# Kernel optimization log

Hardware: AMD Instinct MI355X
Metric: run time of the kernel (lower is better)

The kernel has to match this reference:

```python
import jax, jax.numpy as jnp
import numpy as np

BLOCK = 64
THRESH = 0.95
EPS = 1e-8


def setup_inputs() -> dict:
    key = jax.random.key(0)
    kq, kk, kv = jax.random.split(key, 3)
    S, D = 4096, 128
    q = jax.random.normal(kq, (S, D), dtype=jnp.float32)
    k = jax.random.normal(kk, (S, D), dtype=jnp.float32)
    v = jax.random.normal(kv, (S, D), dtype=jnp.float32)
    return {"q": q, "k": k, "v": v}


def reference(q, k, v):
    S, D = q.shape
    nb = S // BLOCK
    qb = q.reshape(nb, BLOCK, D)
    kb = k.reshape(nb, BLOCK, D)
    vb = v.reshape(nb, BLOCK, D)
    # all block-pair scores: [nb_q, nb_k, BLOCK_q, BLOCK_k]
    scores = jnp.einsum('ibd,jcd->ijbc', qb, kb)
    m = jnp.max(scores, axis=-1, keepdims=True)
    e = jnp.exp(scores - m)
    s = jnp.sum(e, axis=-1, keepdims=True)  # per-block-pair softmax denominator
    # top-p truncation mask: sort descending, cumsum, threshold
    srt = jnp.sort(e, axis=-1)[..., ::-1]
    cum = jnp.cumsum(srt, axis=-1)
    mask = cum < THRESH * s
    # NOTE: faithful to original — mask (in sorted order) is applied to the
    # UNSORTED exp_scores, exactly as the torch code does (indices unused).
    em = e * mask
    em = em / (jnp.sum(em, axis=-1, keepdims=True) + EPS)
    # accumulate over key blocks j (per-pair normalized weights, summed)
    out = jnp.einsum('ijbc,jcd->ibd', em, vb)
    return out.reshape(S, D)
```

## Files before the change

kernel.cpp:

```cpp
#include <hip/hip_runtime.h>
#include <cstdint>
#include <cstddef>


#define SEQ   4096
#define DIM   128
#define BLK   64
#define NB    (SEQ / BLK)
#define NJG   16
#define JPB   (NB / NJG)
#define NT    256
#define PSTR  12288
#define THRESH 0.95f
#define EPSF   1e-8f

typedef __attribute__((ext_vector_type(8))) _Float16 f16x8;
typedef __attribute__((ext_vector_type(4))) float    f32x4;

#define MFMAH(a, b, c) __builtin_amdgcn_mfma_f32_16x16x32_f16((a), (b), (c), 0, 0, 0)

union UH4 { uint2 u; _Float16 h[4]; };
union UH8 { uint4 u; f16x8 v; };

__device__ __forceinline__ void gll16(const uint* g, uint* l) {
  __builtin_amdgcn_global_load_lds(
      (const __attribute__((address_space(1))) void*)g,
      (__attribute__((address_space(3))) void*)l, 16, 0, 0);
}

__global__ __launch_bounds__(NT, 4) void eco_prep_kernel(
    const float* __restrict__ K, const float* __restrict__ V,
    uint* __restrict__ P, float* __restrict__ O) {
  const int tid  = threadIdx.x;
  const int b    = blockIdx.x;
  const int jb   = b >> 2;
  const int part = b & 3;

  {
    float4 z = {0.f, 0.f, 0.f, 0.f};
    float4* op = (float4*)O;
#pragma unroll
    for (int it = 0; it < 2; ++it) op[b * 512 + it * NT + tid] = z;
  }

  {
    const float4* gk = (const float4*)(K + (size_t)jb * BLK * DIM);
    uint* dst = P + (size_t)jb * PSTR;
#pragma unroll
    for (int it = 0; it < 2; ++it) {
      int f = part * 512 + it * NT + tid;
      int r = f >> 5, c4 = f & 31;
      float4 x = gk[f];
      float xs[4] = {x.x, x.y, x.z, x.w};
      UH4 uh, ur;
#pragma unroll
      for (int e = 0; e < 4; ++e) {
        float v = xs[e];
        _Float16 h = (_Float16)v;
        uh.h[e] = h;
        ur.h[e] = (_Float16)(v - (float)h);
      }
      uint off = (uint)r * 64u + (((uint)(c4 >> 1) ^ (uint)(r & 15)) << 2) +
                 (uint)((c4 & 1) << 1);
      *(uint2*)&dst[off]        = uh.u;
      *(uint2*)&dst[4096 + off] = ur.u;
    }
  }

  {
    const float* gv = V + (size_t)jb * BLK * DIM;
    uint4* dv = (uint4*)(P + (size_t)jb * PSTR + 8192);
    int idx = part * 256 + tid;
    int ch = idx >> 7, d = idx & 127;
    UH8 u;
#pragma unroll
    for (int j = 0; j < 8; ++j)
      u.v[j] = (_Float16)gv[(ch * 8 + j) * DIM + d];
    dv[idx] = u.u;
  }
}

#define CE(x, y, dmax) { float _hi = fmaxf((x), (y)); float _lo = fminf((x), (y)); \
                         (x) = (dmax) ? _hi : _lo; (y) = (dmax) ? _lo : _hi; }

__global__ __launch_bounds__(NT, 4) void eco_attn_kernel(
    const float* __restrict__ Q, const uint* __restrict__ P,
    float* __restrict__ O) {
  __shared__ __align__(16) uint sK[8192];
  __shared__ __align__(16) uint sW[2048];

  const int tid  = threadIdx.x;
  const int ib   = blockIdx.y;
  const int jg   = blockIdx.x;
  const int lane = tid & 63;
  const int wv   = tid >> 6;
  const int quad = lane >> 4;
  const int l16  = lane & 15;
  const int q4   = quad << 2;

  uint* sWw = sW + wv * 512;

  f16x8 qh[4], qr[4];
  {
    const float* qp = Q + (size_t)(ib * BLK + wv * 16 + l16) * DIM + quad * 8;
#pragma unroll
    for (int ks = 0; ks < 4; ++ks) {
      float4 x0 = *(const float4*)(qp + ks * 32);
      float4 x1 = *(const float4*)(qp + ks * 32 + 4);
      float xs[8] = {x0.x, x0.y, x0.z, x0.w, x1.x, x1.y, x1.z, x1.w};
      f16x8 h8, r8;
#pragma unroll
      for (int e = 0; e < 8; ++e) {
        float v = xs[e];
        _Float16 h = (_Float16)v;
        h8[e] = h;
        r8[e] = (_Float16)(v - (float)h);
      }
      qh[ks] = h8; qr[ks] = r8;
    }
  }

  const f32x4 zf = {0.f, 0.f, 0.f, 0.f};
  f32x4 pv[8];
#pragma unroll
  for (int i = 0; i < 8; ++i) pv[i] = zf;

  {
    const uint* gsrc = P + (size_t)(jg * JPB) * PSTR;
#pragma unroll
    for (int it = 0; it < 8; ++it) {
      int idx = (it * NT + tid) << 2;
      gll16(gsrc + idx, sK + idx);
    }
  }

  for (int jj = 0; jj < JPB; ++jj) {
    const int jb = jg * JPB + jj;
    __syncthreads();

    f32x4 ah[4], ar[4];
#pragma unroll
    for (int nt = 0; nt < 4; ++nt) { ah[nt] = zf; ar[nt] = zf; }
#pragma unroll
    for (int nt = 0; nt < 4; ++nt) {
      const int rB = nt * 16 + l16;
      const uint rowoff = (uint)rB * 64u;
      const uint swk = (uint)(rB & 15);
#pragma unroll
      for (int ks = 0; ks < 4; ++ks) {
        uint off = rowoff + ((((uint)(ks * 4 + quad)) ^ swk) << 2);
        f16x8 bh = *(const f16x8*)&sK[off];
        f16x8 br = *(const f16x8*)&sK[4096 + off];
        ah[nt] = MFMAH(bh, qh[ks], ah[nt]);
        ar[nt] = MFMAH(br, qh[ks], ar[nt]);
        ar[nt] = MFMAH(bh, qr[ks], ar[nt]);
      }
    }
    __syncthreads();

    if (jj + 1 < JPB) {
      const uint* gsrc = P + (size_t)(jb + 1) * PSTR;
#pragma unroll
      for (int it = 0; it < 8; ++it) {
        int idx = (it * NT + tid) << 2;
        gll16(gsrc + idx, sK + idx);
      }
    }

    bool doHi;

    {
      float a[16], e[16];
#pragma unroll
      for (int nt = 0; nt < 4; ++nt) {
        f32x4 sc = ah[nt] + ar[nt];
#pragma unroll
        for (int rg = 0; rg < 4; ++rg) a[nt * 4 + rg] = sc[rg];
      }
      float mt[8];
#pragma unroll
      for (int i = 0; i < 8; ++i) mt[i] = fmaxf(a[i], a[i + 8]);
#pragma unroll
      for (int w2 = 4; w2 >= 1; w2 >>= 1)
#pragma unroll
        for (int i = 0; i < w2; ++i) mt[i] = fmaxf(mt[i], mt[i + w2]);
      float m = mt[0];
      m = fmaxf(m, __shfl_xor(m, 16, 64));
      m = fmaxf(m, __shfl_xor(m, 32, 64));
#pragma unroll
      for (int i = 0; i < 16; ++i) { a[i] = __expf(a[i] - m); e[i] = a[i]; }
      float st[8];
#pragma unroll
      for (int i = 0; i < 8; ++i) st[i] = a[i] + a[i + 8];
#pragma unroll
      for (int w2 = 4; w2 >= 1; w2 >>= 1)
#pragma unroll
        for (int i = 0; i < w2; ++i) st[i] += st[i + w2];
      float sr = st[0];
      sr += __shfl_xor(sr, 16, 64);
      sr += __shfl_xor(sr, 32, 64);
      const float T = THRESH * sr;

      float cum = 1.0f;
      bool live = (cum < T);
      int t = live ? 1 : 0;
#pragma unroll
      for (int i = 0; i < 16; ++i) a[i] = (a[i] >= 1.0f) ? 0.f : a[i];
#pragma unroll
      for (int p4 = 0; p4 < 4; ++p4) {
        float M = fmaxf(fmaxf(fmaxf(a[0], a[1]), a[2]),
                        fmaxf(fmaxf(a[3], a[4]), a[5]));
        M = fmaxf(M, fmaxf(fmaxf(a[6],  a[7]),  a[8]));
        M = fmaxf(M, fmaxf(fmaxf(a[9],  a[10]), a[11]));
        M = fmaxf(M, fmaxf(fmaxf(a[12], a[13]), a[14]));
        M = fmaxf(M, a[15]);
        M = fmaxf(M, __shfl_xor(M, 16, 64));
        M = fmaxf(M, __shfl_xor(M, 32, 64));
        const float cn = cum + M;
        const bool cross = !(cn < T) || !(M > 0.f);
        if (live) { cum = cn; t += cross ? 0 : 1; }
        live = live && !cross;
#pragma unroll
        for (int i = 0; i < 16; ++i) a[i] = (a[i] >= M) ? 0.f : a[i];
      }

      if (__any(live)) {
        const int s = quad;
#pragma unroll
        for (int k2 = 2; k2 <= 8; k2 <<= 1)
#pragma unroll
          for (int j2 = k2 >> 1; j2 >= 1; j2 >>= 1)
#pragma unroll
            for (int i = 0; i < 16; ++i) {
              int l = i ^ j2;
              if (l > i) { bool d = ((i & k2) == 0); CE(a[i], a[l], d); }
            }
        const bool x16 = ((s & 1) == 0);
        const bool x32 = ((s & 2) == 0);
#pragma unroll
        for (int j2 = 8; j2 >= 1; j2 >>= 1)
#pragma unroll
          for (int i = 0; i < 16; ++i) {
            int l = i ^ j2;
            if (l > i) { CE(a[i], a[l], x16); }
          }
        {
          const bool km = (x32 == x16);
#pragma unroll
          for (int i = 0; i < 16; ++i) {
            float o = __shfl_xor(a[i], 16, 64);
            a[i] = km ? fmaxf(a[i], o) : fminf(a[i], o);
          }
#pragma unroll
          for (int j2 = 8; j2 >= 1; j2 >>= 1)
#pragma unroll
            for (int i = 0; i < 16; ++i) {
              int l = i ^ j2;
              if (l > i) { CE(a[i], a[l], x32); }
            }
        }
        {
#pragma unroll
          for (int i = 0; i < 16; ++i) {
            float o = __shfl_xor(a[i], 32, 64);
            a[i] = x32 ? fmaxf(a[i], o) : fminf(a[i], o);
          }
#pragma unroll
          for (int i = 0; i < 16; ++i) {
            float o = __shfl_xor(a[i], 16, 64);
            a[i] = x16 ? fmaxf(a[i], o) : fminf(a[i], o);
          }
#pragma unroll
          for (int j2 = 8; j2 >= 1; j2 >>= 1)
#pragma unroll
            for (int i = 0; i < 16; ++i) {
              int l = i ^ j2;
              if (l > i) { CE(a[i], a[l], true); }
            }
        }
#pragma unroll
        for (int i = 1; i < 16; ++i) a[i] += a[i - 1];
        float tot = a[15];
        float c = tot;
        float o1 = __shfl_up(c, 16, 64); if (s >= 1) c += o1;
        float o2 = __shfl_up(c, 32, 64); if (s >= 2) c += o2;
        const float excl = c - tot;
        int cnt = 0;
#pragma unroll
        for (int i = 0; i < 16; ++i) cnt += ((cum + a[i] + excl) < T) ? 1 : 0;
        cnt += __shfl_xor(cnt, 16, 64);
        cnt += __shfl_xor(cnt, 32, 64);
        if (live) t += cnt;
      }

      {
        int tm = t;
        int o;
        o = __shfl_xor(tm, 1, 64); tm = (o > tm) ? o : tm;
        o = __shfl_xor(tm, 2, 64); tm = (o > tm) ? o : tm;
        o = __shfl_xor(tm, 4, 64); tm = (o > tm) ? o : tm;
        o = __shfl_xor(tm, 8, 64); tm = (o > tm) ? o : tm;
        doHi = (tm > 32);
      }

      float p = 0.f;
#pragma unroll
      for (int i = 0; i < 16; ++i) {
        int kidx = ((i >> 2) << 4) + q4 + (i & 3);
        p += (kidx < t) ? e[i] : 0.f;
      }
      p += __shfl_xor(p, 16, 64);
      p += __shfl_xor(p, 32, 64);
      const float rn = 1.0f / (p + EPSF);
      uint* wrow = sWw + l16 * 32;
#pragma unroll
      for (int nt = 0; nt < 2; ++nt) {
        UH4 u;
#pragma unroll
        for (int rg = 0; rg < 4; ++rg) {
          int kidx = nt * 16 + q4 + rg;
          float w = (kidx < t) ? e[nt * 4 + rg] * rn : 0.f;
          u.h[rg] = (_Float16)w;
        }
        uint c4 = (uint)(nt * 4 + quad);
        *(uint2*)&wrow[(c4 ^ (uint)l16) << 1] = u.u;
      }
      if (doHi) {
#pragma unroll
        for (int nt = 2; nt < 4; ++nt) {
          UH4 u;
#pragma unroll
          for (int rg = 0; rg < 4; ++rg) {
            int kidx = nt * 16 + q4 + rg;
            float w = (kidx < t) ? e[nt * 4 + rg] * rn : 0.f;
            u.h[rg] = (_Float16)w;
          }
          uint c4 = (uint)(nt * 4 + quad);
          *(uint2*)&wrow[(c4 ^ (uint)l16) << 1] = u.u;
        }
      }
    }
    __builtin_amdgcn_wave_barrier();

    const uint* gvt = P + (size_t)jb * PSTR + 8192;
    {
      uint c0 = (uint)(quad * 2);
      const uint* wrow = sWw + l16 * 32;
      uint2 lo = *(const uint2*)&wrow[(c0 ^ (uint)l16) << 1];
      uint2 hi = *(const uint2*)&wrow[((c0 + 1) ^ (uint)l16) << 1];
      UH8 u;
      u.u = make_uint4(lo.x, lo.y, hi.x, hi.y);
      f16x8 wf0 = u.v;
#pragma unroll
      for (int nt2 = 0; nt2 < 8; ++nt2) {
        f16x8 vf = *(const f16x8*)&gvt[((uint)(quad * 128 +
                                               nt2 * 16 + l16)) << 2];
        pv[nt2] = MFMAH(wf0, vf, pv[nt2]);
      }
    }
    if (doHi) {
      uint c0 = (uint)(8 + quad * 2);
      const uint* wrow = sWw + l16 * 32;
      uint2 lo = *(const uint2*)&wrow[(c0 ^ (uint)l16) << 1];
      uint2 hi = *(const uint2*)&wrow[((c0 + 1) ^ (uint)l16) << 1];
      UH8 u;
      u.u = make_uint4(lo.x, lo.y, hi.x, hi.y);
      f16x8 wf1 = u.v;
#pragma unroll
      for (int nt2 = 0; nt2 < 8; ++nt2) {
        f16x8 vf = *(const f16x8*)&gvt[((uint)((4 + quad) * 128 +
                                               nt2 * 16 + l16)) << 2];
        pv[nt2] = MFMAH(wf1, vf, pv[nt2]);
      }
    }
  }

#pragma unroll
  for (int nt2 = 0; nt2 < 8; ++nt2) {
    const int col  = nt2 * 16 + l16;
    const int row0 = ib * BLK + wv * 16 + quad * 4;
#pragma unroll
    for (int rg = 0; rg < 4; ++rg)
      atomicAdd(O + (size_t)(row0 + rg) * DIM + col, pv[nt2][rg]);
  }
}

extern "C" void kernel_launch(void* const* d_in, const int* in_sizes, int n_in,
                              void* d_out, int out_size, void* d_ws, size_t ws_size,
                              hipStream_t stream) {
  (void)in_sizes; (void)n_in; (void)ws_size; (void)out_size;
  const float* q = (const float*)d_in[0];
  const float* k = (const float*)d_in[1];
  const float* v = (const float*)d_in[2];
  float* out = (float*)d_out;
  uint* prep = (uint*)d_ws;

  eco_prep_kernel<<<dim3(NB * 4), dim3(NT), 0, stream>>>(k, v, prep, out);
  eco_attn_kernel<<<dim3(NJG, NB), dim3(NT), 0, stream>>>(q, prep, out);
}
```

Baseline: 116.4 us.

## Replace output atomics with per-group partial buffers and a reduction kernel

The attention kernel now writes each key-group's partial output to its own workspace slice instead of issuing float atomicAdds into the output, and a new kernel sums the 16 partials. The prep kernel is also re-gridded into 16 smaller blocks per key block, with only 192 of 256 threads doing work. The goal is to avoid atomic contention and the read-modify-write traffic on the output. In exchange it adds about 32 MB of partial writes and reads plus an extra kernel launch. The new path runs only when the workspace is large enough.

```diff
diff --git a/kernel.cpp b/kernel.cpp
--- a/kernel.cpp
+++ b/kernel.cpp
@@ -13,6 +13,9 @@
 #define PSTR  12288
 #define THRESH 0.95f
 #define EPSF   1e-8f
+#define PPART  (PSTR * NB)
+#define PARTF  (NJG * SEQ * DIM)
+#define WS_NEED ((size_t)PPART * 4 + (size_t)PARTF * 4)
 
 typedef __attribute__((ext_vector_type(8))) _Float16 f16x8;
 typedef __attribute__((ext_vector_type(4))) float    f32x4;
@@ -31,46 +34,37 @@
 __global__ __launch_bounds__(NT, 4) void eco_prep_kernel(
     const float* __restrict__ K, const float* __restrict__ V,
     uint* __restrict__ P, float* __restrict__ O) {
-  const int tid  = threadIdx.x;
-  const int b    = blockIdx.x;
-  const int jb   = b >> 2;
-  const int part = b & 3;
-
-  {
+  const int tid = threadIdx.x;
+  const int w   = blockIdx.x;
+  const int jb  = w >> 4;
+  const int sub = w & 15;
+
+  if (tid < 128) {
     float4 z = {0.f, 0.f, 0.f, 0.f};
-    float4* op = (float4*)O;
-#pragma unroll
-    for (int it = 0; it < 2; ++it) op[b * 512 + it * NT + tid] = z;
-  }
-
-  {
+    ((float4*)O)[w * 128 + tid] = z;
+
     const float4* gk = (const float4*)(K + (size_t)jb * BLK * DIM);
     uint* dst = P + (size_t)jb * PSTR;
-#pragma unroll
-    for (int it = 0; it < 2; ++it) {
-      int f = part * 512 + it * NT + tid;
-      int r = f >> 5, c4 = f & 31;
-      float4 x = gk[f];
-      float xs[4] = {x.x, x.y, x.z, x.w};
-      UH4 uh, ur;
-#pragma unroll
-      for (int e = 0; e < 4; ++e) {
-        float v = xs[e];
-        _Float16 h = (_Float16)v;
-        uh.h[e] = h;
-        ur.h[e] = (_Float16)(v - (float)h);
-      }
-      uint off = (uint)r * 64u + (((uint)(c4 >> 1) ^ (uint)(r & 15)) << 2) +
-                 (uint)((c4 & 1) << 1);
-      *(uint2*)&dst[off]        = uh.u;
-      *(uint2*)&dst[4096 + off] = ur.u;
-    }
-  }
-
-  {
+    int f = sub * 128 + tid;
+    int r = f >> 5, c4 = f & 31;
+    float4 x = gk[f];
+    float xs[4] = {x.x, x.y, x.z, x.w};
+    UH4 uh, ur;
+#pragma unroll
+    for (int e = 0; e < 4; ++e) {
+      float v = xs[e];
+      _Float16 h = (_Float16)v;
+      uh.h[e] = h;
+      ur.h[e] = (_Float16)(v - (float)h);
+    }
+    uint off = (uint)r * 64u + (((uint)(c4 >> 1) ^ (uint)(r & 15)) << 2) +
+               (uint)((c4 & 1) << 1);
+    *(uint2*)&dst[off]        = uh.u;
+    *(uint2*)&dst[4096 + off] = ur.u;
+  } else if (tid < 192) {
     const float* gv = V + (size_t)jb * BLK * DIM;
     uint4* dv = (uint4*)(P + (size_t)jb * PSTR + 8192);
-    int idx = part * 256 + tid;
+    int idx = sub * 64 + (tid - 128);
     int ch = idx >> 7, d = idx & 127;
     UH8 u;
 #pragma unroll
@@ -80,12 +74,26 @@
   }
 }
 
+__global__ __launch_bounds__(NT) void eco_reduce_kernel(
+    const float* __restrict__ Part, float* __restrict__ O) {
+  const int gid = blockIdx.x * NT + threadIdx.x;
+  const float4* p4 = (const float4*)Part;
+  float4 a = p4[gid];
+#pragma unroll
+  for (int jg = 1; jg < NJG; ++jg) {
+    float4 b = p4[(size_t)jg * (SEQ * DIM / 4) + gid];
+    a.x += b.x; a.y += b.y; a.z += b.z; a.w += b.w;
+  }
+  ((float4*)O)[gid] = a;
+}
+
 #define CE(x, y, dmax) { float _hi = fmaxf((x), (y)); float _lo = fminf((x), (y)); \
                          (x) = (dmax) ? _hi : _lo; (y) = (dmax) ? _lo : _hi; }
 
+template <bool PARTIAL>
 __global__ __launch_bounds__(NT, 4) void eco_attn_kernel(
     const float* __restrict__ Q, const uint* __restrict__ P,
-    float* __restrict__ O) {
+    float* __restrict__ O, float* __restrict__ Part) {
   __shared__ __align__(16) uint sK[8192];
   __shared__ __align__(16) uint sW[2048];
 
@@ -375,26 +383,44 @@
     }
   }
 
-#pragma unroll
-  for (int nt2 = 0; nt2 < 8; ++nt2) {
-    const int col  = nt2 * 16 + l16;
+  if constexpr (PARTIAL) {
+    float* pb = Part + (size_t)jg * (SEQ * DIM);
     const int row0 = ib * BLK + wv * 16 + quad * 4;
 #pragma unroll
-    for (int rg = 0; rg < 4; ++rg)
-      atomicAdd(O + (size_t)(row0 + rg) * DIM + col, pv[nt2][rg]);
+    for (int nt2 = 0; nt2 < 8; ++nt2) {
+      const int col = nt2 * 16 + l16;
+#pragma unroll
+      for (int rg = 0; rg < 4; ++rg)
+        pb[(size_t)(row0 + rg) * DIM + col] = pv[nt2][rg];
+    }
+  } else {
+#pragma unroll
+    for (int nt2 = 0; nt2 < 8; ++nt2) {
+      const int col  = nt2 * 16 + l16;
+      const int row0 = ib * BLK + wv * 16 + quad * 4;
+#pragma unroll
+      for (int rg = 0; rg < 4; ++rg)
+        atomicAdd(O + (size_t)(row0 + rg) * DIM + col, pv[nt2][rg]);
+    }
   }
 }
 
 extern "C" void kernel_launch(void* const* d_in, const int* in_sizes, int n_in,
                               void* d_out, int out_size, void* d_ws, size_t ws_size,
                               hipStream_t stream) {
-  (void)in_sizes; (void)n_in; (void)ws_size; (void)out_size;
+  (void)in_sizes; (void)n_in; (void)out_size;
   const float* q = (const float*)d_in[0];
   const float* k = (const float*)d_in[1];
   const float* v = (const float*)d_in[2];
   float* out = (float*)d_out;
   uint* prep = (uint*)d_ws;
-
-  eco_prep_kernel<<<dim3(NB * 4), dim3(NT), 0, stream>>>(k, v, prep, out);
-  eco_attn_kernel<<<dim3(NJG, NB), dim3(NT), 0, stream>>>(q, prep, out);
+  float* part = (float*)((char*)d_ws + (size_t)PPART * 4);
+
+  eco_prep_kernel<<<dim3(NB * 16), dim3(NT), 0, stream>>>(k, v, prep, out);
+  if (ws_size >= WS_NEED) {
+    eco_attn_kernel<true><<<dim3(NJG, NB), dim3(NT), 0, stream>>>(q, prep, out, part);
+    eco_reduce_kernel<<<dim3(SEQ * DIM / 4 / NT), dim3(NT), 0, stream>>>(part, out);
+  } else {
+    eco_attn_kernel<false><<<dim3(NJG, NB), dim3(NT), 0, stream>>>(q, prep, out, nullptr);
+  }
 }
```

After: 114.9 us. Within noise of the previous version (-1.3%).
